# Performance work log

Measured on AMD Instinct MI355X. Metric: run time of the kernel, lower is better.

## Reference

```python
import jax, jax.numpy as jnp
import numpy as np
from jax import lax

SEQ, FEAT, U1, U2, U3, OUT = 20, 5, 10, 7, 4, 4
BATCH = 262144


def _he_uniform(key, shape, fan_in):
    lim = np.sqrt(6.0 / fan_in)
    return jax.random.uniform(key, shape, jnp.float32, -lim, lim)


def _orthogonal(key, n, m):
    a = jax.random.normal(key, (max(n, m), min(n, m)), jnp.float32)
    q, _ = jnp.linalg.qr(a)
    return q[:n, :m] if n >= m else q[:m, :n].T


def _lstm_params(key, in_dim, units):
    k1, k2 = jax.random.split(key)
    Wk = _he_uniform(k1, (in_dim, 4 * units), in_dim)
    Wr = _orthogonal(k2, units, 4 * units)
    # Keras unit_forget_bias: bias = [zeros(i), ones(f), zeros(c), zeros(o)]
    b = jnp.concatenate([jnp.zeros(units), jnp.ones(units), jnp.zeros(2 * units)]).astype(jnp.float32)
    return Wk, Wr, b


def setup_inputs() -> dict:
    key = jax.random.key(0)
    ks = jax.random.split(key, 5)
    x = jax.random.normal(ks[0], (BATCH, SEQ, FEAT), jnp.float32)
    Wk1, Wr1, b1 = _lstm_params(ks[1], FEAT, U1)
    Wk2, Wr2, b2 = _lstm_params(ks[2], U1, U2)
    Wk3, Wr3, b3 = _lstm_params(ks[3], U2, U3)
    kd1, kd2 = jax.random.split(ks[4])
    lim = np.sqrt(6.0 / (U3 + OUT))  # glorot_uniform (Dense default)
    Wd = jax.random.uniform(kd1, (U3, OUT), jnp.float32, -lim, lim)
    bd = jnp.zeros((OUT,), jnp.float32)
    return {"x": x, "Wk1": Wk1, "Wr1": Wr1, "b1": b1,
            "Wk2": Wk2, "Wr2": Wr2, "b2": b2,
            "Wk3": Wk3, "Wr3": Wr3, "b3": b3,
            "Wd": Wd, "bd": bd}


def lstm_layer(x, Wk, Wr, b):
    # x: [B, T, F] -> h-sequence [B, T, U]; Keras gate order i, f, c(g), o
    B = x.shape[0]
    U = Wr.shape[0]
    # precompute input projection for all timesteps (one big GEMM)
    zx = jnp.einsum('btf,fg->btg', x, Wk) + b  # [B, T, 4U]
    zxT = jnp.swapaxes(zx, 0, 1)               # [T, B, 4U]

    def step(carry, zt):
        h, c = carry
        z = zt + h @ Wr
        i, f, g, o = jnp.split(z, 4, axis=-1)
        i = jax.nn.sigmoid(i)
        f = jax.nn.sigmoid(f)
        g = jnp.tanh(g)
        o = jax.nn.sigmoid(o)
        c = f * c + i * g
        h = o * jnp.tanh(c)
        return (h, c), h

    init = (jnp.zeros((B, U), x.dtype), jnp.zeros((B, U), x.dtype))
    _, hs = lax.scan(step, init, zxT)
    return jnp.swapaxes(hs, 0, 1)  # [B, T, U]


def reference(x, Wk1, Wr1, b1, Wk2, Wr2, b2, Wk3, Wr3, b3, Wd, bd):
    h = lstm_layer(x, Wk1, Wr1, b1)
    h = lstm_layer(h, Wk2, Wr2, b2)
    h = lstm_layer(h, Wk3, Wr3, b3)
    return jax.nn.sigmoid(jnp.einsum('btu,uo->bto', h, Wd) + bd)
```

## Files before the change

### kernel.cpp

```cpp
#include <hip/hip_runtime.h>

static constexpr int SEQ = 20, FEAT = 5, NU1 = 10, NU2 = 7, NU3 = 4, NOUT = 4;

typedef short bf16x8 __attribute__((ext_vector_type(8)));
typedef float f32x4  __attribute__((ext_vector_type(4)));


__device__ __forceinline__ unsigned short bf16_hi_rne(float x) {
    unsigned u = __float_as_uint(x);
    return (unsigned short)((u + 0x7FFF + ((u >> 16) & 1)) >> 16);
}
__device__ __forceinline__ unsigned short bf16_trunc(float x) {
    return (unsigned short)(__float_as_uint(x) >> 16);
}
__device__ __forceinline__ float bf16_to_f(unsigned short h) {
    return __uint_as_float(((unsigned)h) << 16);
}
__device__ __forceinline__ unsigned hpack(float h) {
    unsigned u = __float_as_uint(h);
    unsigned r = (u + 0x7FFF + ((u >> 16) & 1)) >> 16;
    unsigned lo = __float_as_uint(h - __uint_as_float(r << 16)) >> 16;
    return r | (lo << 16);
}

__device__ __forceinline__ float sigm(float x) {
    return __builtin_amdgcn_rcpf(1.0f + __builtin_amdgcn_exp2f(x * -1.4426950408889634f));
}
__device__ __forceinline__ float ftanh(float x) {
    return 1.0f - 2.0f * __builtin_amdgcn_rcpf(1.0f + __builtin_amdgcn_exp2f(x * 2.8853900817779268f));
}

__device__ __forceinline__ unsigned act_unit(const f32x4 z, float& c) {
    float gi = sigm(z[0]), gf = sigm(z[1]), gg = ftanh(z[2]), go = sigm(z[3]);
    c = gf * c + gi * gg;
    return hpack(go * ftanh(c));
}

__device__ __forceinline__ unsigned bperm(int idx, unsigned v) {
    return (unsigned)__builtin_amdgcn_ds_bpermute(idx, (int)v);
}
__device__ __forceinline__ bf16x8 bfrag(unsigned v0, unsigned v1) {
    uint4 u{v0, v0, v1, v1};
    return __builtin_bit_cast(bf16x8, u);
}

__global__ void build_afrags(const float* Wk1, const float* Wr1, const float* b1,
                             const float* Wk2, const float* Wr2, const float* b2,
                             const float* Wk3, const float* Wr3, const float* b3,
                             const float* Wd,  const float* bd, unsigned* ws) {
    const int lane = threadIdx.x;
    const int Us[3] = {NU1, NU2, NU3};
    const int nF[3] = {10, 10, 7};
    const int nS[3] = {5, 7, 4};
    const float* Fm[3] = {Wr1, Wk2, Wk3};
    const float* Sm[3] = {Wk1, Wr2, Wr3};
    const float* Bs[3] = {b1, b2, b3};
    const int baseid[3] = {0, 6, 12}, KT[3] = {2, 3, 2}, MT[3] = {3, 2, 1};
    for (int L = 0; L < 3; ++L) {
        const int U = Us[L], nf = nF[L], ns = nS[L];
        const int Itot = nf + ns;
        for (int tau = 0; tau < MT[L]; ++tau)
        for (int kap = 0; kap < KT[L]; ++kap) {
            const int id = baseid[L] + tau * KT[L] + kap;
            unsigned short h8[8];
            for (int j = 0; j < 8; ++j) {
                const int m = lane & 15;
                const int k = kap * 32 + (lane >> 4) * 8 + j;
                const int i = k >> 2, cls = k & 3;
                const int u = tau * 4 + (m >> 2), g = m & 3, col = g * U + u;
                unsigned short v = 0;
                if (u < U && i <= Itot) {
                    float W = (i < nf)   ? Fm[L][i * 4 * U + col]
                            : (i < Itot) ? Sm[L][(i - nf) * 4 * U + col]
                                         : Bs[L][col];
                    unsigned short hi = bf16_hi_rne(W);
                    v = (cls < 2) ? hi : bf16_trunc(W - bf16_to_f(hi));
                }
                h8[j] = v;
            }
            for (int d = 0; d < 4; ++d)
                ws[id * 256 + lane * 4 + d] = (unsigned)h8[2 * d] | ((unsigned)h8[2 * d + 1] << 16);
        }
    }
    {
        unsigned short h8[8];
        for (int j = 0; j < 8; ++j) {
            const int m = lane & 15;
            const int k = (lane >> 4) * 8 + j;
            const int i = k >> 2, cls = k & 3;
            unsigned short v = 0;
            if (m < NOUT && i <= 4) {
                float W = (i < 4) ? Wd[i * NOUT + m] : bd[m];
                unsigned short hi = bf16_hi_rne(W);
                v = (cls < 2) ? hi : bf16_trunc(W - bf16_to_f(hi));
            }
            h8[j] = v;
        }
        for (int d = 0; d < 4; ++d)
            ws[14 * 256 + lane * 4 + d] = (unsigned)h8[2 * d] | ((unsigned)h8[2 * d + 1] << 16);
    }
}

__global__ __launch_bounds__(256, 4) void lstm3_mfma(
    const float* __restrict__ x, const unsigned* __restrict__ wsA,
    float* __restrict__ out, int B) {
    const int tid = threadIdx.x;
    const int lane = tid & 63;
    const int n = lane & 15;
    const int q = lane >> 4;

    bf16x8 af[15];
#pragma unroll
    for (int i = 0; i < 15; ++i) {
        uint4 v = ((const uint4*)wsA)[i * 64 + lane];
        af[i] = __builtin_bit_cast(bf16x8, v);
    }

    const int ie  = (n + 16 * ((2 * q) & 3))     << 2;
    const int io  = (n + 16 * ((2 * q + 1) & 3)) << 2;
    const int ie2 = (n + 16 * ((2 * q + 2) & 3)) << 2;
    const int io2 = (n + 16 * ((2 * q + 3) & 3)) << 2;
    const int in0 = n << 2, in1 = (n + 16) << 2, in2 = (n + 32) << 2;

    const f32x4 zro = {0.f, 0.f, 0.f, 0.f};

    const int ngrp = B >> 4;
    const int gw = (blockIdx.x * blockDim.x + tid) >> 6;
    const int nw = (gridDim.x * blockDim.x) >> 6;

    for (int grp = gw; grp < ngrp; grp += nw) {
        const float* xr = x + (size_t)grp * 16 * (SEQ * FEAT) + n * (SEQ * FEAT);
        float* ob = out + (size_t)grp * 16 * (SEQ * NOUT) + n * (SEQ * NOUT);

        unsigned p1a = 0, p1b = 0, p1c = 0, p2a = 0, p2b = 0, p3 = 0;
        unsigned F0v0 = 0, F0v1 = 0, tC0 = 0, tC1 = 0;
        float c10 = 0.f, c11 = 0.f, c12 = 0.f, c20 = 0.f, c21 = 0.f, c30 = 0.f;

        float xa = 0.f, xc = 0.f;
        if (q != 0) {
            const float* p = xr + 2 * (q - 1);
            xa = p[0];
            if (q != 3) xc = p[1];
        }

#pragma unroll 1
        for (int t = 0; t < SEQ; ++t) {
            unsigned xP0 = hpack(xa), xP1 = hpack(xc);
            {
                const int tn = (t + 1 < SEQ) ? t + 1 : 0;
                if (q != 0) {
                    const float* p = xr + tn * FEAT + 2 * (q - 1);
                    xa = p[0];
                    if (q != 3) xc = p[1];
                }
            }
            unsigned F1v0 = (q == 0) ? tC0 : xP0;
            unsigned F1v1 = (q == 0) ? tC1 : ((q == 3) ? 0x3F80u : xP1);

            f32x4 z0 = __builtin_amdgcn_mfma_f32_16x16x32_bf16(af[0], bfrag(F0v0, F0v1), zro, 0, 0, 0);
            z0 = __builtin_amdgcn_mfma_f32_16x16x32_bf16(af[1], bfrag(F1v0, F1v1), z0, 0, 0, 0);
            f32x4 z1 = __builtin_amdgcn_mfma_f32_16x16x32_bf16(af[2], bfrag(F0v0, F0v1), zro, 0, 0, 0);
            z1 = __builtin_amdgcn_mfma_f32_16x16x32_bf16(af[3], bfrag(F1v0, F1v1), z1, 0, 0, 0);
            f32x4 z2 = __builtin_amdgcn_mfma_f32_16x16x32_bf16(af[4], bfrag(F0v0, F0v1), zro, 0, 0, 0);
            z2 = __builtin_amdgcn_mfma_f32_16x16x32_bf16(af[5], bfrag(F1v0, F1v1), z2, 0, 0, 0);
            p1a = act_unit(z0, c10);
            p1b = act_unit(z1, c11);
            p1c = act_unit(z2, c12);

            {
                unsigned ae = bperm(ie, p1a), be = bperm(ie, p1b);
                unsigned ao = bperm(io, p1a), bo = bperm(io, p1b);
                F0v0 = (q < 2) ? ae : be;
                F0v1 = (q < 2) ? ao : bo;
                tC0 = bperm(in0, p1c);
                tC1 = bperm(in1, p1c);
            }
            unsigned F2v0, F2v1, F3v0;
            {
                unsigned de = bperm(ie2, p2a), ee = bperm(ie2, p2b);
                unsigned dd = bperm(io2, p2a), eo = bperm(io2, p2b);
                F2v0 = (q == 0) ? tC0 : ((q < 3) ? de : ee);
                F2v1 = (q == 0) ? tC1 : ((q < 3) ? dd : eo);
                F3v0 = bperm(in2, p2b);
            }
            const unsigned F3v1 = 0x3F80u;

            f32x4 y0 = __builtin_amdgcn_mfma_f32_16x16x32_bf16(af[6], bfrag(F0v0, F0v1), zro, 0, 0, 0);
            y0 = __builtin_amdgcn_mfma_f32_16x16x32_bf16(af[7], bfrag(F2v0, F2v1), y0, 0, 0, 0);
            y0 = __builtin_amdgcn_mfma_f32_16x16x32_bf16(af[8], bfrag(F3v0, F3v1), y0, 0, 0, 0);
            f32x4 y1 = __builtin_amdgcn_mfma_f32_16x16x32_bf16(af[9], bfrag(F0v0, F0v1), zro, 0, 0, 0);
            y1 = __builtin_amdgcn_mfma_f32_16x16x32_bf16(af[10], bfrag(F2v0, F2v1), y1, 0, 0, 0);
            y1 = __builtin_amdgcn_mfma_f32_16x16x32_bf16(af[11], bfrag(F3v0, F3v1), y1, 0, 0, 0);
            p2a = act_unit(y0, c20);
            p2b = act_unit(y1, c21);

            unsigned F4v0, F4v1, F5v0, F5v1;
            {
                unsigned ge = bperm(ie, p2a), he = bperm(ie, p2b);
                unsigned go = bperm(io, p2a), ho = bperm(io, p2b);
                unsigned pp0 = bperm(in0, p3);
                F4v0 = (q < 2) ? ge : he;
                F4v1 = (q < 2) ? go : ((q == 2) ? ho : pp0);
                F5v0 = bperm(io, p3);
                F5v1 = (q == 1) ? 0x3F80u : bperm(in2, p3);
            }
            f32x4 w0 = __builtin_amdgcn_mfma_f32_16x16x32_bf16(af[12], bfrag(F4v0, F4v1), zro, 0, 0, 0);
            w0 = __builtin_amdgcn_mfma_f32_16x16x32_bf16(af[13], bfrag(F5v0, F5v1), w0, 0, 0, 0);
            p3 = act_unit(w0, c30);

            unsigned F6v0, F6v1;
            {
                unsigned ue = bperm(ie, p3), uo = bperm(io, p3);
                F6v0 = (q == 2) ? 0x3F80u : ue;
                F6v1 = uo;
            }
            f32x4 o0 = __builtin_amdgcn_mfma_f32_16x16x32_bf16(af[14], bfrag(F6v0, F6v1), zro, 0, 0, 0);
            if (q == 0) {
                float4 o4;
                o4.x = sigm(o0[0]); o4.y = sigm(o0[1]);
                o4.z = sigm(o0[2]); o4.w = sigm(o0[3]);
                *(float4*)(ob + t * NOUT) = o4;
            }
        }
    }
}

extern "C" void kernel_launch(void* const* d_in, const int* in_sizes, int n_in,
                              void* d_out, int out_size, void* d_ws, size_t ws_size,
                              hipStream_t stream) {
    const float* x   = (const float*)d_in[0];
    const float* Wk1 = (const float*)d_in[1];
    const float* Wr1 = (const float*)d_in[2];
    const float* b1  = (const float*)d_in[3];
    const float* Wk2 = (const float*)d_in[4];
    const float* Wr2 = (const float*)d_in[5];
    const float* b2  = (const float*)d_in[6];
    const float* Wk3 = (const float*)d_in[7];
    const float* Wr3 = (const float*)d_in[8];
    const float* b3  = (const float*)d_in[9];
    const float* Wd  = (const float*)d_in[10];
    const float* bd  = (const float*)d_in[11];
    float* out = (float*)d_out;
    unsigned* ws = (unsigned*)d_ws;

    const int B = in_sizes[0] / (SEQ * FEAT);

    build_afrags<<<1, 64, 0, stream>>>(Wk1, Wr1, b1, Wk2, Wr2, b2,
                                       Wk3, Wr3, b3, Wd, bd, ws);
    lstm3_mfma<<<2048, 256, 0, stream>>>(x, ws, out, B);
}
```

Measured before the change: 392.9 us.

## Permute weight fragment rows to cut cross-lane permutes and use hardware bf16 pack

```diff
diff --git a/kernel.cpp b/kernel.cpp
--- a/kernel.cpp
+++ b/kernel.cpp
@@ -17,10 +17,10 @@
     return __uint_as_float(((unsigned)h) << 16);
 }
 __device__ __forceinline__ unsigned hpack(float h) {
-    unsigned u = __float_as_uint(h);
-    unsigned r = (u + 0x7FFF + ((u >> 16) & 1)) >> 16;
-    unsigned lo = __float_as_uint(h - __uint_as_float(r << 16)) >> 16;
-    return r | (lo << 16);
+    unsigned rp;
+    asm("v_cvt_pk_bf16_f32 %0, %1, %1" : "=v"(rp) : "v"(h));
+    float lo = h - __uint_as_float(rp << 16);
+    return __builtin_amdgcn_perm(__float_as_uint(lo), rp, 0x07060100u);
 }
 
 __device__ __forceinline__ float sigm(float x) {
@@ -49,50 +49,107 @@
                              const float* Wk3, const float* Wr3, const float* b3,
                              const float* Wd,  const float* bd, unsigned* ws) {
     const int lane = threadIdx.x;
-    const int Us[3] = {NU1, NU2, NU3};
-    const int nF[3] = {10, 10, 7};
-    const int nS[3] = {5, 7, 4};
-    const float* Fm[3] = {Wr1, Wk2, Wk3};
-    const float* Sm[3] = {Wk1, Wr2, Wr3};
-    const float* Bs[3] = {b1, b2, b3};
-    const int baseid[3] = {0, 6, 12}, KT[3] = {2, 3, 2}, MT[3] = {3, 2, 1};
-    for (int L = 0; L < 3; ++L) {
-        const int U = Us[L], nf = nF[L], ns = nS[L];
-        const int Itot = nf + ns;
-        for (int tau = 0; tau < MT[L]; ++tau)
-        for (int kap = 0; kap < KT[L]; ++kap) {
-            const int id = baseid[L] + tau * KT[L] + kap;
-            unsigned short h8[8];
-            for (int j = 0; j < 8; ++j) {
-                const int m = lane & 15;
-                const int k = kap * 32 + (lane >> 4) * 8 + j;
-                const int i = k >> 2, cls = k & 3;
-                const int u = tau * 4 + (m >> 2), g = m & 3, col = g * U + u;
-                unsigned short v = 0;
-                if (u < U && i <= Itot) {
-                    float W = (i < nf)   ? Fm[L][i * 4 * U + col]
-                            : (i < Itot) ? Sm[L][(i - nf) * 4 * U + col]
-                                         : Bs[L][col];
+    const int m = lane & 15;
+    const int qh = lane >> 4;
+
+    for (int tau = 0; tau < 3; ++tau)
+    for (int kap = 0; kap < 2; ++kap) {
+        unsigned short h8[8];
+        for (int j = 0; j < 8; ++j) {
+            const int k = kap * 32 + qh * 8 + j;
+            const int i = k >> 2, cls = k & 3;
+            const int u = tau * 4 + (m >> 2), col = (m & 3) * NU1 + u;
+            unsigned short v = 0;
+            if (u < NU1) {
+                if (i < 15) {
+                    float W;
+                    if (i < 8)       W = Wr1[((i >> 1) + 4 * (i & 1)) * 40 + col];
+                    else if (i < 10) W = Wr1[i * 40 + col];
+                    else             W = Wk1[(i - 10) * 40 + col];
                     unsigned short hi = bf16_hi_rne(W);
                     v = (cls < 2) ? hi : bf16_trunc(W - bf16_to_f(hi));
-                }
-                h8[j] = v;
-            }
-            for (int d = 0; d < 4; ++d)
-                ws[id * 256 + lane * 4 + d] = (unsigned)h8[2 * d] | ((unsigned)h8[2 * d + 1] << 16);
-        }
-    }
-    {
-        unsigned short h8[8];
-        for (int j = 0; j < 8; ++j) {
-            const int m = lane & 15;
-            const int k = (lane >> 4) * 8 + j;
-            const int i = k >> 2, cls = k & 3;
-            unsigned short v = 0;
-            if (m < NOUT && i <= 4) {
-                float W = (i < 4) ? Wd[i * NOUT + m] : bd[m];
+                } else if (i == 15) {
+                    float bv = b1[col];
+                    unsigned short hi = bf16_hi_rne(bv);
+                    v = (cls == 0) ? hi : ((cls == 1) ? bf16_trunc(bv - bf16_to_f(hi)) : (unsigned short)0);
+                }
+            }
+            h8[j] = v;
+        }
+        const int id = tau * 2 + kap;
+        for (int d = 0; d < 4; ++d)
+            ws[id * 256 + lane * 4 + d] = (unsigned)h8[2 * d] | ((unsigned)h8[2 * d + 1] << 16);
+    }
+    for (int tau = 0; tau < 2; ++tau)
+    for (int kap = 0; kap < 3; ++kap) {
+        unsigned short h8[8];
+        for (int j = 0; j < 8; ++j) {
+            const int k = kap * 32 + qh * 8 + j;
+            const int i = k >> 2, cls = k & 3;
+            const int u = tau * 4 + (m >> 2), col = (m & 3) * NU2 + u;
+            unsigned short v = 0;
+            if (u < NU2) {
+                if (i < 17) {
+                    float W;
+                    if (i < 8)        W = Wk2[((i >> 1) + 4 * (i & 1)) * 28 + col];
+                    else if (i < 10)  W = Wk2[i * 28 + col];
+                    else if (i < 16)  W = Wr2[(((i - 10) >> 1) + 4 * ((i - 10) & 1)) * 28 + col];
+                    else              W = Wr2[3 * 28 + col];
+                    unsigned short hi = bf16_hi_rne(W);
+                    v = (cls < 2) ? hi : bf16_trunc(W - bf16_to_f(hi));
+                } else if (i == 17) {
+                    float bv = b2[col];
+                    unsigned short hi = bf16_hi_rne(bv);
+                    v = (cls == 0) ? hi : ((cls == 1) ? bf16_trunc(bv - bf16_to_f(hi)) : (unsigned short)0);
+                }
+            }
+            h8[j] = v;
+        }
+        const int id = 6 + tau * 3 + kap;
+        for (int d = 0; d < 4; ++d)
+            ws[id * 256 + lane * 4 + d] = (unsigned)h8[2 * d] | ((unsigned)h8[2 * d + 1] << 16);
+    }
+    for (int kap = 0; kap < 2; ++kap) {
+        unsigned short h8[8];
+        for (int j = 0; j < 8; ++j) {
+            const int k = kap * 32 + qh * 8 + j;
+            const int i = k >> 2, cls = k & 3;
+            const int u = m >> 2, col = (m & 3) * NU3 + u;
+            unsigned short v = 0;
+            if (i < 11) {
+                float W;
+                if (i < 6)       W = Wk3[((i >> 1) + 4 * (i & 1)) * 16 + col];
+                else if (i == 6) W = Wk3[3 * 16 + col];
+                else             W = Wr3[(i - 7) * 16 + col];
                 unsigned short hi = bf16_hi_rne(W);
                 v = (cls < 2) ? hi : bf16_trunc(W - bf16_to_f(hi));
+            } else if (i == 11) {
+                float bv = b3[col];
+                unsigned short hi = bf16_hi_rne(bv);
+                v = (cls == 0) ? hi : ((cls == 1) ? bf16_trunc(bv - bf16_to_f(hi)) : (unsigned short)0);
+            }
+            h8[j] = v;
+        }
+        const int id = 12 + kap;
+        for (int d = 0; d < 4; ++d)
+            ws[id * 256 + lane * 4 + d] = (unsigned)h8[2 * d] | ((unsigned)h8[2 * d + 1] << 16);
+    }
+    {
+        unsigned short h8[8];
+        for (int j = 0; j < 8; ++j) {
+            const int k = qh * 8 + j;
+            const int i = k >> 2, cls = k & 3;
+            unsigned short v = 0;
+            if (m < NOUT) {
+                if (i < 4) {
+                    float W = Wd[i * NOUT + m];
+                    unsigned short hi = bf16_hi_rne(W);
+                    v = (cls < 2) ? hi : bf16_trunc(W - bf16_to_f(hi));
+                } else if (i == 4) {
+                    float bv = bd[m];
+                    unsigned short hi = bf16_hi_rne(bv);
+                    v = (cls == 0) ? hi : ((cls == 1) ? bf16_trunc(bv - bf16_to_f(hi)) : (unsigned short)0);
+                }
             }
             h8[j] = v;
         }
@@ -116,12 +173,12 @@
         af[i] = __builtin_bit_cast(bf16x8, v);
     }
 
-    const int ie  = (n + 16 * ((2 * q) & 3))     << 2;
-    const int io  = (n + 16 * ((2 * q + 1) & 3)) << 2;
-    const int ie2 = (n + 16 * ((2 * q + 2) & 3)) << 2;
-    const int io2 = (n + 16 * ((2 * q + 3) & 3)) << 2;
-    const int in0 = n << 2, in1 = (n + 16) << 2, in2 = (n + 32) << 2;
-
+    const int i_h19 = (n + 16) << 2;
+    const int i_sh  = (n + 16 * ((q + 3) & 3)) << 2;
+    const int i_r1  = (n + 16 * ((q + 1) & 3)) << 2;
+    const int i_r2  = (n + 16 * ((q + 2) & 3)) << 2;
+
+    const unsigned ONE = 0x3F803F80u;
     const f32x4 zro = {0.f, 0.f, 0.f, 0.f};
 
     const int ngrp = B >> 4;
@@ -132,8 +189,8 @@
         const float* xr = x + (size_t)grp * 16 * (SEQ * FEAT) + n * (SEQ * FEAT);
         float* ob = out + (size_t)grp * 16 * (SEQ * NOUT) + n * (SEQ * NOUT);
 
-        unsigned p1a = 0, p1b = 0, p1c = 0, p2a = 0, p2b = 0, p3 = 0;
-        unsigned F0v0 = 0, F0v1 = 0, tC0 = 0, tC1 = 0;
+        unsigned p1a = 0, p1b = 0, p1c = 0, t9 = 0;
+        unsigned p2a = 0, p2b = 0, p3 = 0, rot = 0, rot2 = 0;
         float c10 = 0.f, c11 = 0.f, c12 = 0.f, c20 = 0.f, c21 = 0.f, c30 = 0.f;
 
         float xa = 0.f, xc = 0.f;
@@ -145,7 +202,7 @@
 
 #pragma unroll 1
         for (int t = 0; t < SEQ; ++t) {
-            unsigned xP0 = hpack(xa), xP1 = hpack(xc);
+            const unsigned xP0 = hpack(xa), xP1 = hpack(xc);
             {
                 const int tn = (t + 1 < SEQ) ? t + 1 : 0;
                 if (q != 0) {
@@ -154,66 +211,46 @@
                     if (q != 3) xc = p[1];
                 }
             }
-            unsigned F1v0 = (q == 0) ? tC0 : xP0;
-            unsigned F1v1 = (q == 0) ? tC1 : ((q == 3) ? 0x3F80u : xP1);
-
-            f32x4 z0 = __builtin_amdgcn_mfma_f32_16x16x32_bf16(af[0], bfrag(F0v0, F0v1), zro, 0, 0, 0);
-            z0 = __builtin_amdgcn_mfma_f32_16x16x32_bf16(af[1], bfrag(F1v0, F1v1), z0, 0, 0, 0);
-            f32x4 z1 = __builtin_amdgcn_mfma_f32_16x16x32_bf16(af[2], bfrag(F0v0, F0v1), zro, 0, 0, 0);
-            z1 = __builtin_amdgcn_mfma_f32_16x16x32_bf16(af[3], bfrag(F1v0, F1v1), z1, 0, 0, 0);
-            f32x4 z2 = __builtin_amdgcn_mfma_f32_16x16x32_bf16(af[4], bfrag(F0v0, F0v1), zro, 0, 0, 0);
-            z2 = __builtin_amdgcn_mfma_f32_16x16x32_bf16(af[5], bfrag(F1v0, F1v1), z2, 0, 0, 0);
+            bf16x8 bF0 = bfrag(p1a, p1b);
+            unsigned F1v0 = (q == 0) ? p1c : xP0;
+            unsigned F1v1 = (q == 0) ? t9 : ((q == 3) ? ONE : xP1);
+            bf16x8 bF1 = bfrag(F1v0, F1v1);
+            f32x4 z0 = __builtin_amdgcn_mfma_f32_16x16x32_bf16(af[0], bF0, zro, 0, 0, 0);
+            z0 = __builtin_amdgcn_mfma_f32_16x16x32_bf16(af[1], bF1, z0, 0, 0, 0);
+            f32x4 z1 = __builtin_amdgcn_mfma_f32_16x16x32_bf16(af[2], bF0, zro, 0, 0, 0);
+            z1 = __builtin_amdgcn_mfma_f32_16x16x32_bf16(af[3], bF1, z1, 0, 0, 0);
+            f32x4 z2 = __builtin_amdgcn_mfma_f32_16x16x32_bf16(af[4], bF0, zro, 0, 0, 0);
+            z2 = __builtin_amdgcn_mfma_f32_16x16x32_bf16(af[5], bF1, z2, 0, 0, 0);
+            const unsigned s2a = bperm(i_sh, p2a);
+            const unsigned s2b = bperm(i_sh, p2b);
             p1a = act_unit(z0, c10);
             p1b = act_unit(z1, c11);
             p1c = act_unit(z2, c12);
-
-            {
-                unsigned ae = bperm(ie, p1a), be = bperm(ie, p1b);
-                unsigned ao = bperm(io, p1a), bo = bperm(io, p1b);
-                F0v0 = (q < 2) ? ae : be;
-                F0v1 = (q < 2) ? ao : bo;
-                tC0 = bperm(in0, p1c);
-                tC1 = bperm(in1, p1c);
-            }
-            unsigned F2v0, F2v1, F3v0;
-            {
-                unsigned de = bperm(ie2, p2a), ee = bperm(ie2, p2b);
-                unsigned dd = bperm(io2, p2a), eo = bperm(io2, p2b);
-                F2v0 = (q == 0) ? tC0 : ((q < 3) ? de : ee);
-                F2v1 = (q == 0) ? tC1 : ((q < 3) ? dd : eo);
-                F3v0 = bperm(in2, p2b);
-            }
-            const unsigned F3v1 = 0x3F80u;
-
-            f32x4 y0 = __builtin_amdgcn_mfma_f32_16x16x32_bf16(af[6], bfrag(F0v0, F0v1), zro, 0, 0, 0);
-            y0 = __builtin_amdgcn_mfma_f32_16x16x32_bf16(af[7], bfrag(F2v0, F2v1), y0, 0, 0, 0);
-            y0 = __builtin_amdgcn_mfma_f32_16x16x32_bf16(af[8], bfrag(F3v0, F3v1), y0, 0, 0, 0);
-            f32x4 y1 = __builtin_amdgcn_mfma_f32_16x16x32_bf16(af[9], bfrag(F0v0, F0v1), zro, 0, 0, 0);
-            y1 = __builtin_amdgcn_mfma_f32_16x16x32_bf16(af[10], bfrag(F2v0, F2v1), y1, 0, 0, 0);
-            y1 = __builtin_amdgcn_mfma_f32_16x16x32_bf16(af[11], bfrag(F3v0, F3v1), y1, 0, 0, 0);
+            t9  = bperm(i_h19, p1c);
+            bf16x8 bA  = bfrag(p1a, p1b);
+            unsigned F2v0 = (q == 0) ? p1c : s2a;
+            unsigned F2v1 = (q == 0) ? t9  : s2b;
+            bf16x8 bF2 = bfrag(F2v0, F2v1);
+            bf16x8 bF3 = bfrag(s2a, ONE);
+            f32x4 y0 = __builtin_amdgcn_mfma_f32_16x16x32_bf16(af[6], bA, zro, 0, 0, 0);
+            y0 = __builtin_amdgcn_mfma_f32_16x16x32_bf16(af[7], bF2, y0, 0, 0, 0);
+            y0 = __builtin_amdgcn_mfma_f32_16x16x32_bf16(af[8], bF3, y0, 0, 0, 0);
+            f32x4 y1 = __builtin_amdgcn_mfma_f32_16x16x32_bf16(af[9], bA, zro, 0, 0, 0);
+            y1 = __builtin_amdgcn_mfma_f32_16x16x32_bf16(af[10], bF2, y1, 0, 0, 0);
+            y1 = __builtin_amdgcn_mfma_f32_16x16x32_bf16(af[11], bF3, y1, 0, 0, 0);
             p2a = act_unit(y0, c20);
             p2b = act_unit(y1, c21);
-
-            unsigned F4v0, F4v1, F5v0, F5v1;
-            {
-                unsigned ge = bperm(ie, p2a), he = bperm(ie, p2b);
-                unsigned go = bperm(io, p2a), ho = bperm(io, p2b);
-                unsigned pp0 = bperm(in0, p3);
-                F4v0 = (q < 2) ? ge : he;
-                F4v1 = (q < 2) ? go : ((q == 2) ? ho : pp0);
-                F5v0 = bperm(io, p3);
-                F5v1 = (q == 1) ? 0x3F80u : bperm(in2, p3);
-            }
-            f32x4 w0 = __builtin_amdgcn_mfma_f32_16x16x32_bf16(af[12], bfrag(F4v0, F4v1), zro, 0, 0, 0);
-            w0 = __builtin_amdgcn_mfma_f32_16x16x32_bf16(af[13], bfrag(F5v0, F5v1), w0, 0, 0, 0);
+            bf16x8 bF4 = bfrag(p2a, (q == 3) ? rot : p2b);
+            unsigned F5v0 = (q == 0) ? rot  : rot2;
+            unsigned F5v1 = (q == 0) ? rot2 : ONE;
+            bf16x8 bF5 = bfrag(F5v0, F5v1);
+            f32x4 w0 = __builtin_amdgcn_mfma_f32_16x16x32_bf16(af[12], bF4, zro, 0, 0, 0);
+            w0 = __builtin_amdgcn_mfma_f32_16x16x32_bf16(af[13], bF5, w0, 0, 0, 0);
             p3 = act_unit(w0, c30);
-
-            unsigned F6v0, F6v1;
-            {
-                unsigned ue = bperm(ie, p3), uo = bperm(io, p3);
-                F6v0 = (q == 2) ? 0x3F80u : ue;
-                F6v1 = uo;
-            }
+            rot  = bperm(i_r1, p3);
+            rot2 = bperm(i_r2, p3);
+            unsigned F6v0 = (q == 0) ? p3 : ((q == 1) ? rot : ONE);
+            unsigned F6v1 = (q == 0) ? rot : rot2;
             f32x4 o0 = __builtin_amdgcn_mfma_f32_16x16x32_bf16(af[14], bfrag(F6v0, F6v1), zro, 0, 0, 0);
             if (q == 0) {
                 float4 o4;
```

Result: no change. 386.2 us (-1.7%).
